# Performance work log

Measured on AMD Instinct MI355X. Metric: run time of the kernel, lower is better.

The kernel has to match this reference:

```python
import jax, jax.numpy as jnp
import numpy as np

B = 8
IN_FEATURES = 8192
OUT_FEATURES = 8192


def setup_inputs() -> dict:
    key = jax.random.key(0)
    k_x, k_w, k_b = jax.random.split(key, 3)
    x = jax.random.normal(k_x, (B, IN_FEATURES), dtype=jnp.float32)
    # kaiming-uniform-like init for weight [out, in]
    bound_w = np.sqrt(6.0 / IN_FEATURES)  # approx kaiming_uniform with a=sqrt(5)
    weight = jax.random.uniform(k_w, (OUT_FEATURES, IN_FEATURES), dtype=jnp.float32,
                                minval=-bound_w, maxval=bound_w)
    bound_b = 1.0 / np.sqrt(IN_FEATURES)
    bias = jax.random.uniform(k_b, (OUT_FEATURES,), dtype=jnp.float32,
                              minval=-bound_b, maxval=bound_b)
    return {"input": x, "weight": weight, "bias": bias}


def reference(input, weight, bias):
    # Ternary (sign) quantize both operands, then GEMV per batch row:
    # out[b, o] = sum_i sign(x[b, i]) * sign(W[o, i])  (+ bias)
    x_t = jnp.sign(input)            # [B, in] in {-1, 0, +1}
    w_t = jnp.sign(weight)           # [out, in] in {-1, 0, +1}
    out = jnp.einsum('bi,oi->bo', x_t, w_t)  # [B, out]
    return out + bias
```

## Files before the change

### kernel.cpp

```cpp
#include <hip/hip_runtime.h>
#include <stdint.h>

#define IN_F 8192
#define OUT_F 8192
#define BATCH 8
#define XWORDS (BATCH * IN_F / 32)

__global__ void pack_sign_kernel(const uint32_t* __restrict__ x,
                                 uint32_t* __restrict__ xbits) {
  int i = blockIdx.x * blockDim.x + threadIdx.x;
  uint32_t neg = x[i] >> 31;
  unsigned long long m = __ballot(neg != 0);
  int lane = threadIdx.x & 63;
  if (lane == 0) {
    int w = i >> 5;
    xbits[w] = (uint32_t)m;
    xbits[w + 1] = (uint32_t)(m >> 32);
  }
}

__global__ __launch_bounds__(256) void ternary_gemv_kernel(
    const uint4* __restrict__ W, const uint32_t* __restrict__ xbits,
    const float* __restrict__ bias, float* __restrict__ out) {
  __shared__ uint32_t xlds[XWORDS];
  for (int i = threadIdx.x; i < XWORDS; i += 256) xlds[i] = xbits[i];
  __syncthreads();

  const int warp = threadIdx.x >> 6;
  const int lane = threadIdx.x & 63;
  const int row = blockIdx.x * 4 + warp;
  const uint4* wrow = W + (size_t)row * (IN_F / 4);

  int cnt[BATCH] = {0, 0, 0, 0, 0, 0, 0, 0};
  const int shift = (lane & 7) * 4;
  const int wb = lane >> 3;

#pragma unroll 4
  for (int it = 0; it < 32; ++it) {
    uint4 u = wrow[it * 64 + lane];
    uint32_t wn = (u.x >> 31) | ((u.y >> 31) << 1) |
                  ((u.z >> 31) << 2) | ((u.w >> 31) << 3);
    const int widx = it * 8 + wb;
#pragma unroll
    for (int b = 0; b < BATCH; ++b) {
      uint32_t xn = (xlds[b * 256 + widx] >> shift) & 0xFu;
      cnt[b] += __popc(wn ^ xn);
    }
  }

#pragma unroll
  for (int b = 0; b < BATCH; ++b) {
#pragma unroll
    for (int off = 32; off > 0; off >>= 1)
      cnt[b] += __shfl_down(cnt[b], off);
  }

  if (lane == 0) {
    float bv = bias[row];
#pragma unroll
    for (int b = 0; b < BATCH; ++b)
      out[(size_t)b * OUT_F + row] = (float)(IN_F - 2 * cnt[b]) + bv;
  }
}

extern "C" void kernel_launch(void* const* d_in, const int* in_sizes, int n_in,
                              void* d_out, int out_size, void* d_ws, size_t ws_size,
                              hipStream_t stream) {
  const uint32_t* x = (const uint32_t*)d_in[0];
  const uint4* W = (const uint4*)d_in[1];
  const float* bias = (const float*)d_in[2];
  float* out = (float*)d_out;
  uint32_t* xbits = (uint32_t*)d_ws;

  pack_sign_kernel<<<(BATCH * IN_F) / 256, 256, 0, stream>>>(x, xbits);
  ternary_gemv_kernel<<<OUT_F / 4, 256, 0, stream>>>(W, xbits, bias, out);
}
```

Before: 52.51 us.

## Permute packed sign bits to match lane layout and batch weight loads

The input sign-packing kernel now writes x bits in a permuted layout, so each GEMV lane reads one full 32-bit word per batch row instead of shifting and masking 4-bit nibbles. The weight loop now issues 8 nontemporal 16-byte loads before packing them into one 32-bit word, which cuts popcount/XOR and LDS reads by 8x and exposes more memory-level parallelism. The kernel stays memory bound on the 256MB weight stream, so any gain comes mostly from better load issue and bypassing the cache. The cost is higher register pressure from holding eight vector loads at once.

```diff
diff --git a/kernel.cpp b/kernel.cpp
--- a/kernel.cpp
+++ b/kernel.cpp
@@ -4,48 +4,60 @@
 #define IN_F 8192
 #define OUT_F 8192
 #define BATCH 8
-#define XWORDS (BATCH * IN_F / 32)
+#define XPW (BATCH * 4 * 64)
 
-__global__ void pack_sign_kernel(const uint32_t* __restrict__ x,
-                                 uint32_t* __restrict__ xbits) {
-  int i = blockIdx.x * blockDim.x + threadIdx.x;
-  uint32_t neg = x[i] >> 31;
-  unsigned long long m = __ballot(neg != 0);
-  int lane = threadIdx.x & 63;
-  if (lane == 0) {
-    int w = i >> 5;
-    xbits[w] = (uint32_t)m;
-    xbits[w + 1] = (uint32_t)(m >> 32);
+typedef unsigned int u32x4 __attribute__((ext_vector_type(4)));
+
+__global__ __launch_bounds__(256) void pack_sign_perm(
+    const u32x4* __restrict__ x, uint32_t* __restrict__ xp) {
+  const int t = blockIdx.x * 256 + threadIdx.x;
+  const int b = t >> 8;
+  const int m = (t >> 6) & 3;
+  const int l = t & 63;
+  const u32x4* base = x + (b * IN_F + m * 2048 + l * 4) / 4;
+  uint32_t w = 0;
+#pragma unroll
+  for (int i = 0; i < 8; ++i) {
+    u32x4 u = base[i * 64];
+    uint32_t nib = (u.x >> 31) | ((u.y >> 31) << 1) |
+                   ((u.z >> 31) << 2) | ((u.w >> 31) << 3);
+    w |= nib << (4 * i);
   }
+  xp[t] = w;
 }
 
-__global__ __launch_bounds__(256) void ternary_gemv_kernel(
-    const uint4* __restrict__ W, const uint32_t* __restrict__ xbits,
+__global__ __launch_bounds__(256) void ternary_gemv2(
+    const u32x4* __restrict__ W, const uint32_t* __restrict__ xp,
     const float* __restrict__ bias, float* __restrict__ out) {
-  __shared__ uint32_t xlds[XWORDS];
-  for (int i = threadIdx.x; i < XWORDS; i += 256) xlds[i] = xbits[i];
+  __shared__ uint32_t xl[XPW];
+  for (int i = threadIdx.x; i < XPW; i += 256) xl[i] = xp[i];
   __syncthreads();
 
   const int warp = threadIdx.x >> 6;
   const int lane = threadIdx.x & 63;
   const int row = blockIdx.x * 4 + warp;
-  const uint4* wrow = W + (size_t)row * (IN_F / 4);
+  const u32x4* wrow = W + (size_t)row * (IN_F / 4);
 
   int cnt[BATCH] = {0, 0, 0, 0, 0, 0, 0, 0};
-  const int shift = (lane & 7) * 4;
-  const int wb = lane >> 3;
 
-#pragma unroll 4
-  for (int it = 0; it < 32; ++it) {
-    uint4 u = wrow[it * 64 + lane];
-    uint32_t wn = (u.x >> 31) | ((u.y >> 31) << 1) |
-                  ((u.z >> 31) << 2) | ((u.w >> 31) << 3);
-    const int widx = it * 8 + wb;
 #pragma unroll
-    for (int b = 0; b < BATCH; ++b) {
-      uint32_t xn = (xlds[b * 256 + widx] >> shift) & 0xFu;
-      cnt[b] += __popc(wn ^ xn);
+  for (int m = 0; m < 4; ++m) {
+    u32x4 u[8];
+#pragma unroll
+    for (int i = 0; i < 8; ++i)
+      u[i] = __builtin_nontemporal_load(&wrow[m * 512 + i * 64 + lane]);
+
+    uint32_t wn = 0;
+#pragma unroll
+    for (int i = 0; i < 8; ++i) {
+      uint32_t nib = (u[i].x >> 31) | ((u[i].y >> 31) << 1) |
+                     ((u[i].z >> 31) << 2) | ((u[i].w >> 31) << 3);
+      wn |= nib << (4 * i);
     }
+
+#pragma unroll
+    for (int b = 0; b < BATCH; ++b)
+      cnt[b] += __popc(wn ^ xl[(b * 4 + m) * 64 + lane]);
   }
 
 #pragma unroll
@@ -56,7 +68,7 @@
   }
 
   if (lane == 0) {
-    float bv = bias[row];
+    const float bv = bias[row];
 #pragma unroll
     for (int b = 0; b < BATCH; ++b)
       out[(size_t)b * OUT_F + row] = (float)(IN_F - 2 * cnt[b]) + bv;
@@ -66,12 +78,12 @@
 extern "C" void kernel_launch(void* const* d_in, const int* in_sizes, int n_in,
                               void* d_out, int out_size, void* d_ws, size_t ws_size,
                               hipStream_t stream) {
-  const uint32_t* x = (const uint32_t*)d_in[0];
-  const uint4* W = (const uint4*)d_in[1];
+  const u32x4* x = (const u32x4*)d_in[0];
+  const u32x4* W = (const u32x4*)d_in[1];
   const float* bias = (const float*)d_in[2];
   float* out = (float*)d_out;
-  uint32_t* xbits = (uint32_t*)d_ws;
+  uint32_t* xp = (uint32_t*)d_ws;
 
-  pack_sign_kernel<<<(BATCH * IN_F) / 256, 256, 0, stream>>>(x, xbits);
-  ternary_gemv_kernel<<<OUT_F / 4, 256, 0, stream>>>(W, xbits, bias, out);
+  pack_sign_perm<<<XPW / 256, 256, 0, stream>>>(x, xp);
+  ternary_gemv2<<<OUT_F / 4, 256, 0, stream>>>(W, xp, bias, out);
 }
```

Result: faster. 51.00 us (-2.9%).
